# Kernel tuning notes

Measured on AMD Instinct MI355X. Metric: run time of the kernel, lower is better.

The kernel has to match this reference:

```python
import jax, jax.numpy as jnp
import numpy as np

B, T, K, H, NH = 16, 2048, 128, 1024, 8
NEG = -jnp.inf


def _ln(x, g, b, eps=1e-5):
    m = x.mean(-1, keepdims=True)
    v = ((x - m) ** 2).mean(-1, keepdims=True)
    return (x - m) * jax.lax.rsqrt(v + eps) * g + b


def _mha(q, k, v, in_w, in_b, out_w, out_b, nh, bias):
    # torch nn.MultiheadAttention (batch_first, eval mode). bias: additive mask (B or 1, 1, Lq, Lk)
    Bq, Lq, Hd = q.shape
    Lk = k.shape[1]
    d = Hd // nh
    wq, wk, wv = in_w[:Hd], in_w[Hd:2 * Hd], in_w[2 * Hd:]
    bq, bk, bv = in_b[:Hd], in_b[Hd:2 * Hd], in_b[2 * Hd:]
    qh = (q @ wq.T + bq).reshape(Bq, Lq, nh, d).transpose(0, 2, 1, 3)
    kh = (k @ wk.T + bk).reshape(Bq, Lk, nh, d).transpose(0, 2, 1, 3)
    vh = (v @ wv.T + bv).reshape(Bq, Lk, nh, d).transpose(0, 2, 1, 3)
    scores = jnp.einsum('bhqd,bhkd->bhqk', qh, kh) * (1.0 / np.sqrt(d)) + bias
    attn = jax.nn.softmax(scores, axis=-1)
    o = jnp.einsum('bhqk,bhkd->bhqd', attn, vh).transpose(0, 2, 1, 3).reshape(Bq, Lq, Hd)
    return o @ out_w.T + out_b


def setup_inputs() -> dict:
    key = jax.random.key(0)
    ks = jax.random.split(key, 12)
    projected = jax.random.normal(ks[0], (B, T, H), dtype=jnp.float32)
    starts = jnp.sort(jax.random.randint(ks[1], (B, K), 0, T - 1), axis=-1)
    widths = jax.random.randint(ks[2], (B, K), 1, 33)
    ends = jnp.minimum(starts + widths, T)
    boundaries = jnp.stack([starts, ends], axis=-1).astype(jnp.int64)
    slot_mask = jnp.ones((B, K), dtype=jnp.float32)
    s = 0.02
    p = {
        'qp_w': jax.random.normal(ks[3], (H, H)) * s, 'qp_b': jnp.zeros((H,)),
        'ca_in_w': jax.random.normal(ks[4], (3 * H, H)) * s, 'ca_in_b': jnp.zeros((3 * H,)),
        'ca_out_w': jax.random.normal(ks[5], (H, H)) * s, 'ca_out_b': jnp.zeros((H,)),
        'cn_g': jnp.ones((H,)), 'cn_b': jnp.zeros((H,)),
        'sa_in_w': jax.random.normal(ks[6], (3 * H, H)) * s, 'sa_in_b': jnp.zeros((3 * H,)),
        'sa_out_w': jax.random.normal(ks[7], (H, H)) * s, 'sa_out_b': jnp.zeros((H,)),
        'on_g': jnp.ones((H,)), 'on_b': jnp.zeros((H,)),
    }
    return {'projected': projected, 'boundaries': boundaries, 'slot_mask': slot_mask, **p}


def reference(projected, boundaries, slot_mask, qp_w, qp_b, ca_in_w, ca_in_b, ca_out_w, ca_out_b,
              cn_g, cn_b, sa_in_w, sa_in_b, sa_out_w, sa_out_b, on_g, on_b):
    Bb, Tt, Hh = projected.shape
    Kk = slot_mask.shape[1]
    tidx = jnp.arange(Tt)
    starts = boundaries[:, :, 0]  # (B,K)
    ends = boundaries[:, :, 1]
    # in-boundary membership: (B,K,T)
    in_bkt = (tidx[None, None, :] >= starts[:, :, None]) & (tidx[None, None, :] < ends[:, :, None])
    valid = slot_mask > 0.5  # (B,K)
    # --- mean-pool init queries ---
    in_slot = (in_bkt & (slot_mask[:, :, None] > 0)).astype(projected.dtype)  # (B,K,T)
    w = in_slot / jnp.clip(in_slot.sum(axis=-1, keepdims=True), 1.0, None)
    init_slots = jnp.einsum('bkt,bth->bkh', w, projected)
    queries = init_slots @ qp_w.T + qp_b
    # --- boundary-masked cross attention (True = blocked) ---
    blocked = ~(in_bkt & valid[:, :, None])  # (B,K,T)
    cross_bias = jnp.where(blocked, NEG, 0.0)[:, None, :, :]  # (B,1,K,T)
    attn_out = _mha(queries, projected, projected, ca_in_w, ca_in_b, ca_out_w, ca_out_b, NH, cross_bias)
    slots = _ln(attn_out + queries, cn_g, cn_b)
    # --- causal self-attention over slots with key padding ---
    causal = jnp.where(jnp.triu(jnp.ones((Kk, Kk), bool), 1), NEG, 0.0)[None, None, :, :]
    pad = jnp.where(slot_mask[:, None, None, :] < 0.5, NEG, 0.0)  # (B,1,1,K)
    ctx = _mha(slots, slots, slots, sa_in_w, sa_in_b, sa_out_w, sa_out_b, NH, causal + pad)
    return _ln(ctx + slots, on_g, on_b)
```

## Files before the change

kernel.cpp:

```cpp
#include <hip/hip_runtime.h>
#include <hip/hip_bf16.h>


#define Bc 16
#define Tc 2048
#define Kc 128
#define Hc 1024
#define NHc 8

typedef unsigned short u16;
typedef __attribute__((ext_vector_type(8))) short short8v;
typedef __attribute__((ext_vector_type(4))) float f32x4;

__device__ __forceinline__ float bf2f(u16 u){ return __uint_as_float(((unsigned)u)<<16); }
__device__ __forceinline__ u16 f2bf(float f){
  unsigned x = __float_as_uint(f);
  return (u16)((x + 0x7fffu + ((x>>16)&1u)) >> 16);
}
__device__ __forceinline__ float4 ld4(const float* p){ return *(const float4*)p; }
__device__ __forceinline__ float ldx(const void* x, size_t idx, bool isbf){
  return isbf ? bf2f(((const u16*)x)[idx]) : ((const float*)x)[idx];
}
__device__ __forceinline__ bool probe_bf(const u16* probe){ return probe[0] == 0x3F80; }

__device__ __forceinline__ void gload_lds16(const u16* g, u16* l){
  __builtin_amdgcn_global_load_lds(
      (const __attribute__((address_space(1))) unsigned int*)g,
      (__attribute__((address_space(3))) unsigned int*)l, 16, 0, 0);
}

struct CvtArgs { const void* src[15]; int n[15]; long long off[15]; int tobf[15]; };

__global__ __launch_bounds__(256) void convert_params(CvtArgs a, float* fbase,
                                                      u16* bbase, const u16* probe)
{
  bool isbf = probe_bf(probe);
  int g = blockIdx.x*256 + threadIdx.x;
  int stride = gridDim.x*256;
  #pragma unroll 1
  for (int seg=0; seg<15; seg++){
    int n = a.n[seg];
    const void* s = a.src[seg];
    if (a.tobf[seg]){
      u16* d = bbase + a.off[seg];
      if (isbf){ const u16* su=(const u16*)s; for (int i=g;i<n;i+=stride) d[i]=su[i]; }
      else     { const float* sf=(const float*)s; for (int i=g;i<n;i+=stride) d[i]=f2bf(sf[i]); }
    } else {
      float* d = fbase + a.off[seg];
      for (int i=g;i<n;i+=stride) d[i] = ldx(s, i, isbf);
    }
  }
}

__global__ __launch_bounds__(256) void transpose_bf(
    const u16* __restrict__ src, u16* __restrict__ dst, int n)
{
  __shared__ u16 t[32][33];
  int bx = blockIdx.x*32, by = blockIdx.y*32;
  int tx = threadIdx.x & 31, ty = threadIdx.x >> 5;
  #pragma unroll
  for (int i=0;i<32;i+=8)
    t[ty+i][tx] = src[(size_t)(by+ty+i)*n + bx+tx];
  __syncthreads();
  #pragma unroll
  for (int i=0;i<32;i+=8)
    dst[(size_t)(bx+ty+i)*n + by+tx] = t[tx][ty+i];
}

__global__ __launch_bounds__(256) void gemm_mfma(
    const u16* __restrict__ A, const u16* __restrict__ W,
    const float* __restrict__ bias, float* __restrict__ Cf, u16* __restrict__ Cb,
    int M, int N, int Kd, int lda, int ldw, int ldc, float alpha,
    int ZH, long long sAb, long long sAh, long long sWb, long long sWh,
    long long sCb, long long sCh, long long sBh)
{
  __shared__ __align__(16) u16 As[128*32];
  __shared__ __align__(16) u16 Bs[128*32];
  int z = blockIdx.z, bi = z / ZH, hi = z % ZH;
  A += (size_t)bi*sAb + (size_t)hi*sAh;
  W += (size_t)bi*sWb + (size_t)hi*sWh;
  int tid = threadIdx.x;
  int m0 = blockIdx.y*128, n0 = blockIdx.x*128;
  int wave = tid >> 6, lane = tid & 63;
  int wm = (wave >> 1)*64, wn = (wave & 1)*64;
  int r = lane & 15, half = lane >> 4;
  int srow = wave*32 + (lane >> 2);
  int skc  = (lane & 3) << 3;
  u16* ldsA = &As[wave*1024];
  u16* ldsB = &Bs[wave*1024];

  f32x4 acc[4][4] = {};

  for (int k0 = 0; k0 < Kd; k0 += 32){
    gload_lds16(A + (size_t)(m0+srow   )*lda + k0 + skc, ldsA);
    gload_lds16(A + (size_t)(m0+srow+16)*lda + k0 + skc, ldsA + 512);
    gload_lds16(W + (size_t)(n0+srow   )*ldw + k0 + skc, ldsB);
    gload_lds16(W + (size_t)(n0+srow+16)*ldw + k0 + skc, ldsB + 512);
    __syncthreads();
    short8v a[4], b[4];
    #pragma unroll
    for (int mi=0;mi<4;mi++)
      a[mi] = *(const short8v*)&As[(wm+mi*16+r)*32 + half*8];
    #pragma unroll
    for (int ni=0;ni<4;ni++)
      b[ni] = *(const short8v*)&Bs[(wn+ni*16+r)*32 + half*8];
    #pragma unroll
    for (int mi=0;mi<4;mi++)
      #pragma unroll
      for (int ni=0;ni<4;ni++)
        acc[mi][ni] = __builtin_amdgcn_mfma_f32_16x16x32_bf16(a[mi], b[ni], acc[mi][ni], 0, 0, 0);
    __syncthreads();
  }

  float* Cfp = Cf ? Cf + (size_t)bi*sCb + (size_t)hi*sCh : nullptr;
  u16*   Cbp = Cb ? Cb + (size_t)bi*sCb + (size_t)hi*sCh : nullptr;
  #pragma unroll
  for (int ni=0;ni<4;ni++){
    int col = n0 + wn + ni*16 + r;
    float bvv = bias ? bias[(size_t)hi*sBh + col] : 0.f;
    #pragma unroll
    for (int mi=0;mi<4;mi++){
      #pragma unroll
      for (int d=0;d<4;d++){
        int rowc = m0 + wm + mi*16 + half*4 + d;
        float o = alpha*acc[mi][ni][d] + bvv;
        if (Cfp) Cfp[(size_t)rowc*ldc + col] = o;
        if (Cbp) Cbp[(size_t)rowc*ldc + col] = f2bf(o);
      }
    }
  }
}

__global__ __launch_bounds__(256) void gemm_nt(
    const float* __restrict__ A, const float* __restrict__ W,
    const float* __restrict__ bias, float* __restrict__ C,
    int M, int N, int Kd, int lda, int ldw, int ldc, float alpha,
    int ZH, long long sAb, long long sAh, long long sWb, long long sWh,
    long long sCb, long long sCh, long long sBh)
{
  __shared__ float As[16][68];
  __shared__ float Bs[16][68];
  int z = blockIdx.z, bi = z / ZH, hi = z % ZH;
  A += (size_t)bi*sAb + (size_t)hi*sAh;
  W += (size_t)bi*sWb + (size_t)hi*sWh;
  C += (size_t)bi*sCb + (size_t)hi*sCh;
  int tid = threadIdx.x;
  int m0 = blockIdx.y*64, n0 = blockIdx.x*64;
  int tx = tid & 15, ty = tid >> 4;
  int lRow = tid >> 2, lK = (tid & 3) << 2;
  float acc[4][4] = {};
  for (int k0=0; k0<Kd; k0+=16){
    float4 av = ld4(A + (size_t)(m0+lRow)*lda + k0 + lK);
    float4 wv = ld4(W + (size_t)(n0+lRow)*ldw + k0 + lK);
    As[lK+0][lRow]=av.x; As[lK+1][lRow]=av.y; As[lK+2][lRow]=av.z; As[lK+3][lRow]=av.w;
    Bs[lK+0][lRow]=wv.x; Bs[lK+1][lRow]=wv.y; Bs[lK+2][lRow]=wv.z; Bs[lK+3][lRow]=wv.w;
    __syncthreads();
    #pragma unroll
    for (int kk=0;kk<16;kk++){
      float a[4], b[4];
      #pragma unroll
      for (int i=0;i<4;i++) a[i]=As[kk][ty*4+i];
      #pragma unroll
      for (int j=0;j<4;j++) b[j]=Bs[kk][tx*4+j];
      #pragma unroll
      for (int i=0;i<4;i++)
        #pragma unroll
        for (int j=0;j<4;j++)
          acc[i][j] += a[i]*b[j];
    }
    __syncthreads();
  }
  float bv[4] = {0.f,0.f,0.f,0.f};
  if (bias){
    const float* bp = bias + (size_t)hi*sBh + n0 + tx*4;
    bv[0]=bp[0]; bv[1]=bp[1]; bv[2]=bp[2]; bv[3]=bp[3];
  }
  #pragma unroll
  for (int i=0;i<4;i++){
    float4 o;
    o.x = alpha*acc[i][0]+bv[0];
    o.y = alpha*acc[i][1]+bv[1];
    o.z = alpha*acc[i][2]+bv[2];
    o.w = alpha*acc[i][3]+bv[3];
    *(float4*)(C + (size_t)(m0+ty*4+i)*ldc + n0 + tx*4) = o;
  }
}

__global__ __launch_bounds__(256) void gemm_nn(
    const float* __restrict__ A, const float* __restrict__ Bm,
    const float* __restrict__ bias, float* __restrict__ C, u16* __restrict__ Cb,
    int M, int N, int Kd, int lda, int ldb, int ldc, float alpha,
    int ZH, long long sAb, long long sAh, long long sBb, long long sBh,
    long long sCb, long long sCh, long long sBiash)
{
  __shared__ float As[16][68];
  __shared__ float Bs[16][68];
  int z = blockIdx.z, bi = z / ZH, hi = z % ZH;
  A  += (size_t)bi*sAb + (size_t)hi*sAh;
  Bm += (size_t)bi*sBb + (size_t)hi*sBh;
  int tid = threadIdx.x;
  int m0 = blockIdx.y*64, n0 = blockIdx.x*64;
  int tx = tid & 15, ty = tid >> 4;
  int lRow = tid >> 2, lK = (tid & 3) << 2;
  int bKr = tid >> 4, bNc = (tid & 15) << 2;
  float acc[4][4] = {};
  for (int k0=0; k0<Kd; k0+=16){
    float4 av = ld4(A + (size_t)(m0+lRow)*lda + k0 + lK);
    float4 bvv = ld4(Bm + (size_t)(k0+bKr)*ldb + n0 + bNc);
    As[lK+0][lRow]=av.x; As[lK+1][lRow]=av.y; As[lK+2][lRow]=av.z; As[lK+3][lRow]=av.w;
    *(float4*)&Bs[bKr][bNc] = bvv;
    __syncthreads();
    #pragma unroll
    for (int kk=0;kk<16;kk++){
      float a[4], b[4];
      #pragma unroll
      for (int i=0;i<4;i++) a[i]=As[kk][ty*4+i];
      #pragma unroll
      for (int j=0;j<4;j++) b[j]=Bs[kk][tx*4+j];
      #pragma unroll
      for (int i=0;i<4;i++)
        #pragma unroll
        for (int j=0;j<4;j++)
          acc[i][j] += a[i]*b[j];
    }
    __syncthreads();
  }
  float bv[4] = {0.f,0.f,0.f,0.f};
  if (bias){
    const float* bp = bias + (size_t)hi*sBiash + n0 + tx*4;
    bv[0]=bp[0]; bv[1]=bp[1]; bv[2]=bp[2]; bv[3]=bp[3];
  }
  #pragma unroll
  for (int i=0;i<4;i++){
    float o0 = alpha*acc[i][0]+bv[0];
    float o1 = alpha*acc[i][1]+bv[1];
    float o2 = alpha*acc[i][2]+bv[2];
    float o3 = alpha*acc[i][3]+bv[3];
    size_t rowoff = (size_t)(m0+ty*4+i)*ldc + n0 + tx*4;
    if (Cb){
      u16* cp = Cb + (size_t)bi*sCb + (size_t)hi*sCh + rowoff;
      ushort4 ov; ov.x=f2bf(o0); ov.y=f2bf(o1); ov.z=f2bf(o2); ov.w=f2bf(o3);
      *(ushort4*)cp = ov;
    } else {
      float* cp = C + (size_t)bi*sCb + (size_t)hi*sCh + rowoff;
      float4 ov; ov.x=o0; ov.y=o1; ov.z=o2; ov.w=o3;
      *(float4*)cp = ov;
    }
  }
}

__global__ __launch_bounds__(256) void pool_kernel(
    const void* __restrict__ x, const int* __restrict__ bnd,
    const float* __restrict__ maskf, u16* __restrict__ out,
    const u16* __restrict__ probe)
{
  bool isbf = probe_bf(probe);
  bool is64 = (bnd[1] == 0);
  int slot = blockIdx.x; int b = slot >> 7; int tid = threadIdx.x;
  int s0 = is64 ? bnd[4*slot]   : bnd[2*slot];
  int e0 = is64 ? bnd[4*slot+2] : bnd[2*slot+1];
  int d0 = tid*4;
  float acc[4] = {0.f,0.f,0.f,0.f};
  for (int t=s0; t<e0; t++){
    size_t base = ((size_t)b*Tc + (size_t)t)*Hc + d0;
    if (isbf){
      ushort4 v = *(const ushort4*)((const u16*)x + base);
      acc[0]+=bf2f(v.x); acc[1]+=bf2f(v.y); acc[2]+=bf2f(v.z); acc[3]+=bf2f(v.w);
    } else {
      float4 v = ld4((const float*)x + base);
      acc[0]+=v.x; acc[1]+=v.y; acc[2]+=v.z; acc[3]+=v.w;
    }
  }
  int cnt = e0 - s0; if (cnt < 1) cnt = 1;
  float inv = (maskf[slot] > 0.5f) ? 1.f/(float)cnt : 0.f;
  ushort4 o;
  o.x=f2bf(acc[0]*inv); o.y=f2bf(acc[1]*inv); o.z=f2bf(acc[2]*inv); o.w=f2bf(acc[3]*inv);
  *(ushort4*)(out + (size_t)slot*Hc + d0) = o;
}

__global__ __launch_bounds__(512, 2) void cross_attn3(
    const void* __restrict__ x, const int* __restrict__ bnd,
    const u16* __restrict__ Yg, u16* __restrict__ pooled,
    const u16* __restrict__ probe)
{
  __shared__ __align__(16) u16 Xs[32*1024];
  __shared__ float sc[8*32];
  __shared__ __align__(16) float pt[32*8];
  bool isbf = probe_bf(probe);
  bool is64 = (bnd[1] == 0);
  int slot = blockIdx.x; int b = slot >> 7;
  int tid = threadIdx.x;
  int wv = tid >> 6, lane = tid & 63;
  int s0 = is64 ? bnd[4*slot]   : bnd[2*slot];
  int e0 = is64 ? bnd[4*slot+2] : bnd[2*slot+1];
  int w = e0 - s0;

  {
    int rrow = tid >> 7;
    int c = (tid & 127) * 8;
    for (int t = rrow; t < w; t += 4){
      size_t base = ((size_t)b*Tc + (size_t)(s0+t))*Hc + c;
      if (isbf){
        *(short8v*)&Xs[t*1024 + c] = *(const short8v*)((const u16*)x + base);
      } else {
        const float* xf = (const float*)x + base;
        float4 f0 = ld4(xf), f1 = ld4(xf+4);
        short8v v;
        v[0]=(short)f2bf(f0.x); v[1]=(short)f2bf(f0.y);
        v[2]=(short)f2bf(f0.z); v[3]=(short)f2bf(f0.w);
        v[4]=(short)f2bf(f1.x); v[5]=(short)f2bf(f1.y);
        v[6]=(short)f2bf(f1.z); v[7]=(short)f2bf(f1.w);
        *(short8v*)&Xs[t*1024 + c] = v;
      }
    }
  }

  int h = wv;
  float y0[8], y1[8];
  #pragma unroll
  for (int r=0;r<8;r++){
    unsigned yw = *(const unsigned*)(Yg + (size_t)slot*8192 + h*1024 + lane*2 + 128*r);
    y0[r] = bf2f((u16)(yw & 0xffffu));
    y1[r] = bf2f((u16)(yw >> 16));
  }
  __syncthreads();

  const float scale = 0.08838834764831845f;
  for (int t=0; t<w; t++){
    float acc = 0.f;
    #pragma unroll
    for (int r=0;r<8;r++){
      unsigned xw = *(const unsigned*)&Xs[t*1024 + lane*2 + 128*r];
      acc += y0[r]*bf2f((u16)(xw & 0xffffu)) + y1[r]*bf2f((u16)(xw >> 16));
    }
    for (int off=32; off; off>>=1) acc += __shfl_xor(acc, off);
    if (lane==0) sc[h*32 + t] = acc*scale;
  }
  __syncthreads();

  if (tid < 256){
    int hh = tid >> 5, t = tid & 31;
    float v = (t < w) ? sc[hh*32 + t] : -1e30f;
    float m = v;
    for (int off=16; off; off>>=1) m = fmaxf(m, __shfl_xor(m, off));
    float e = (t < w) ? __expf(v - m) : 0.f;
    float s = e;
    for (int off=16; off; off>>=1) s += __shfl_xor(s, off);
    pt[t*8 + hh] = e / s;
  }
  __syncthreads();

  {
    int d0 = tid*2;
    float pa[8][2] = {};
    for (int t=0; t<w; t++){
      float4 p0 = *(const float4*)&pt[t*8];
      float4 p1 = *(const float4*)&pt[t*8+4];
      unsigned xw = *(const unsigned*)&Xs[t*1024 + d0];
      float x0 = bf2f((u16)(xw & 0xffffu));
      float x1 = bf2f((u16)(xw >> 16));
      pa[0][0]+=p0.x*x0; pa[0][1]+=p0.x*x1;
      pa[1][0]+=p0.y*x0; pa[1][1]+=p0.y*x1;
      pa[2][0]+=p0.z*x0; pa[2][1]+=p0.z*x1;
      pa[3][0]+=p0.w*x0; pa[3][1]+=p0.w*x1;
      pa[4][0]+=p1.x*x0; pa[4][1]+=p1.x*x1;
      pa[5][0]+=p1.y*x0; pa[5][1]+=p1.y*x1;
      pa[6][0]+=p1.z*x0; pa[6][1]+=p1.z*x1;
      pa[7][0]+=p1.w*x0; pa[7][1]+=p1.w*x1;
    }
    #pragma unroll
    for (int hh=0;hh<8;hh++){
      ushort2 o; o.x = f2bf(pa[hh][0]); o.y = f2bf(pa[hh][1]);
      *(ushort2*)(pooled + (size_t)slot*8192 + hh*1024 + d0) = o;
    }
  }
}

__global__ __launch_bounds__(256) void ln_res(
    const float* __restrict__ xin, const float* __restrict__ res,
    const float* __restrict__ g, const float* __restrict__ bb,
    float* __restrict__ outf, u16* __restrict__ outb, const u16* __restrict__ probe,
    u16* __restrict__ dualb)
{
  __shared__ float red[256];
  bool tobf = (probe != nullptr) && probe_bf(probe);
  int row = blockIdx.x, tid = threadIdx.x;
  const float* xr = xin + (size_t)row*1024;
  const float* rr = res + (size_t)row*1024;
  float v[4]; float s = 0.f;
  #pragma unroll
  for (int r=0;r<4;r++){ v[r] = xr[tid+256*r] + rr[tid+256*r]; s += v[r]; }
  red[tid] = s; __syncthreads();
  for (int off=128; off>0; off>>=1){ if (tid<off) red[tid]+=red[tid+off]; __syncthreads(); }
  float mean = red[0] * (1.f/1024.f);
  __syncthreads();
  float s2 = 0.f;
  #pragma unroll
  for (int r=0;r<4;r++){ float d = v[r]-mean; s2 += d*d; }
  red[tid]=s2; __syncthreads();
  for (int off=128; off>0; off>>=1){ if (tid<off) red[tid]+=red[tid+off]; __syncthreads(); }
  float var = red[0]*(1.f/1024.f);
  float rs = rsqrtf(var + 1e-5f);
  #pragma unroll
  for (int r=0;r<4;r++){
    int c = tid+256*r;
    float o = (v[r]-mean)*rs*g[c] + bb[c];
    if (tobf) outb[(size_t)row*1024 + c] = f2bf(o);
    else      outf[(size_t)row*1024 + c] = o;
    if (dualb) dualb[(size_t)row*1024 + c] = f2bf(o);
  }
}

__global__ __launch_bounds__(256) void sa_softmax(float* __restrict__ S,
                                                  const float* __restrict__ maskf)
{
  int wv = threadIdx.x>>6, lane = threadIdx.x&63;
  int row = blockIdx.x*4 + wv;
  int z = row >> 7, q = row & 127;
  int b = z >> 3;
  float* Sr = S + (size_t)row*128;
  float v0 = Sr[lane], v1 = Sr[lane+64];
  if (lane    > q || maskf[b*128+lane   ] < 0.5f) v0 = -1e30f;
  if (lane+64 > q || maskf[b*128+lane+64] < 0.5f) v1 = -1e30f;
  float m = fmaxf(v0,v1);
  for (int off=32; off; off>>=1) m = fmaxf(m, __shfl_xor(m,off));
  float e0 = expf(v0-m), e1 = expf(v1-m);
  float s = e0+e1;
  for (int off=32; off; off>>=1) s += __shfl_xor(s,off);
  float inv = 1.f/s;
  Sr[lane] = e0*inv; Sr[lane+64] = e1*inv;
}

extern "C" void kernel_launch(void* const* d_in, const int* in_sizes, int n_in,
                              void* d_out, int out_size, void* d_ws, size_t ws_size,
                              hipStream_t stream)
{
  const void* x       = d_in[0];
  const int* bnd      = (const int*)d_in[1];
  const u16* probe    = (const u16*)d_in[9];
  float* ws = (float*)d_ws;

  const long long F_qp_b    = 0;
  const long long F_ca_in_b = 1024;
  const long long F_ca_out_b= 4096;
  const long long F_cn_g    = 5120;
  const long long F_cn_b    = 6144;
  const long long F_sa_in_b = 7168;
  const long long F_sa_out_b= 10240;
  const long long F_on_g    = 11264;
  const long long F_on_b    = 12288;
  const long long F_smask   = 13312;
  u16* wb = (u16*)(ws + 15360);
  const long long B_qp_w    = 0;
  const long long B_ca_in_w = 1048576;
  const long long B_ca_out_w= 4194304;
  const long long B_sa_in_w = 5242880;
  const long long B_sa_out_w= 8388608;
  const long long B_wkT     = 9437184;
  const long long PB        = 5258240;

  float* qbuf    = ws + PB + 0;
  float* slots   = ws + PB + 2097152;
  u16*   Ybuf    = (u16*)(ws + PB + 4194304);
  u16*   poolb   = Ybuf;
  u16*   islots  = (u16*)(ws + PB + 12582912);
  u16*   qbuf_b  = (u16*)(ws + PB + 13631488);
  u16*   qhbuf   = (u16*)(ws + PB + 14680064);
  u16*   attnb   = (u16*)(ws + PB + 15728640);
  float* attn2   = ws + PB + 16777216;
  u16*   slots_b = (u16*)(ws + PB + 18874368);
  float* qkv     = ws + PB + 19922944;
  float* Sb      = ws + PB + 26214400;
  u16*   ctx_b   = (u16*)(ws + PB + 28311552);
  float* ctx2    = ws + PB + 29360128;
  if (ws_size < (size_t)(PB + 31457280ll) * 4ull) return;

  CvtArgs ca;
  const int srcIdx[15]     = {3,5,7,11,13, 4,6,8,9,10,12,14,15,16, 2};
  const long long offs[15] = {B_qp_w,B_ca_in_w,B_ca_out_w,B_sa_in_w,B_sa_out_w,
                              F_qp_b,F_ca_in_b,F_ca_out_b,F_cn_g,F_cn_b,
                              F_sa_in_b,F_sa_out_b,F_on_g,F_on_b,F_smask};
  const int tobf[15]       = {1,1,1,1,1, 0,0,0,0,0,0,0,0,0, 0};
  for (int i=0;i<15;i++){ ca.src[i]=d_in[srcIdx[i]]; ca.n[i]=in_sizes[srcIdx[i]];
                          ca.off[i]=offs[i]; ca.tobf[i]=tobf[i]; }
  convert_params<<<dim3(4096),dim3(256),0,stream>>>(ca, ws, wb, probe);

  const float* Pf = ws;
  transpose_bf<<<dim3(32,32),dim3(256),0,stream>>>(wb + B_ca_in_w + 1048576ll,
      wb + B_wkT, 1024);
  pool_kernel<<<dim3(2048),dim3(256),0,stream>>>(x, bnd, Pf+F_smask, islots, probe);
  gemm_mfma<<<dim3(8,16,1),dim3(256),0,stream>>>(islots, wb+B_qp_w, Pf+F_qp_b,
      qbuf, qbuf_b,
      2048,1024,1024, 1024,1024,1024, 1.f, 1, 0,0, 0,0, 0,0, 0);
  gemm_mfma<<<dim3(8,16,1),dim3(256),0,stream>>>(qbuf_b, wb+B_ca_in_w, Pf+F_ca_in_b,
      (float*)nullptr, qhbuf,
      2048,1024,1024, 1024,1024,1024, 1.f, 1, 0,0, 0,0, 0,0, 0);
  gemm_mfma<<<dim3(8,16,8),dim3(256),0,stream>>>(qhbuf, wb+B_wkT,
      (const float*)nullptr, (float*)nullptr, Ybuf,
      2048,1024,128, 1024,1024,8192, 1.f, 8, 0,128, 0,128, 0,1024, 0);
  cross_attn3<<<dim3(2048),dim3(512),0,stream>>>(x, bnd, Ybuf, poolb, probe);
  gemm_mfma<<<dim3(1,16,8),dim3(256),0,stream>>>(poolb, wb+B_ca_in_w+2097152ll,
      Pf+F_ca_in_b+2048, (float*)nullptr, attnb,
      2048,128,1024, 8192,1024,1024, 1.f, 8, 0,1024, 0,131072, 0,128, 128);
  gemm_mfma<<<dim3(8,16,1),dim3(256),0,stream>>>(attnb, wb+B_ca_out_w, Pf+F_ca_out_b,
      attn2, (u16*)nullptr,
      2048,1024,1024, 1024,1024,1024, 1.f, 1, 0,0, 0,0, 0,0, 0);
  ln_res<<<dim3(2048),dim3(256),0,stream>>>(attn2, qbuf, Pf+F_cn_g, Pf+F_cn_b,
      slots, (u16*)nullptr, (const u16*)nullptr, slots_b);
  gemm_mfma<<<dim3(24,16,1),dim3(256),0,stream>>>(slots_b, wb+B_sa_in_w, Pf+F_sa_in_b,
      qkv, (u16*)nullptr,
      2048,3072,1024, 1024,1024,3072, 1.f, 1, 0,0, 0,0, 0,0, 0);
  gemm_nt<<<dim3(2,2,128),dim3(256),0,stream>>>(qkv, qkv + 1024,
      (const float*)nullptr, Sb,
      128,128,128, 3072,3072,128, 0.08838834764831845f, 8,
      393216,128, 393216,128, 131072,16384, 0);
  sa_softmax<<<dim3(4096),dim3(256),0,stream>>>(Sb, Pf+F_smask);
  gemm_nn<<<dim3(2,2,128),dim3(256),0,stream>>>(Sb, qkv + 2048,
      (const float*)nullptr, (float*)nullptr, ctx_b,
      128,128,128, 128,3072,1024, 1.f, 8,
      131072,16384, 393216,128, 131072,128, 0);
  gemm_mfma<<<dim3(8,16,1),dim3(256),0,stream>>>(ctx_b, wb+B_sa_out_w, Pf+F_sa_out_b,
      ctx2, (u16*)nullptr,
      2048,1024,1024, 1024,1024,1024, 1.f, 1, 0,0, 0,0, 0,0, 0);
  ln_res<<<dim3(2048),dim3(256),0,stream>>>(ctx2, slots, Pf+F_on_g, Pf+F_on_b,
      (float*)d_out, (u16*)d_out, probe, (u16*)nullptr);
}
```

Before: 567.7 us.

## Compute cross-attention scores with MFMA on swizzled LDS and split pooling rows

New measurement: 538.7 us. 5.1% less time.

```diff
diff --git a/kernel.cpp b/kernel.cpp
--- a/kernel.cpp
+++ b/kernel.cpp
@@ -249,19 +249,21 @@
   }
 }
 
-__global__ __launch_bounds__(256) void pool_kernel(
+__global__ __launch_bounds__(512) void pool_kernel(
     const void* __restrict__ x, const int* __restrict__ bnd,
     const float* __restrict__ maskf, u16* __restrict__ out,
     const u16* __restrict__ probe)
 {
+  __shared__ float red[1024];
   bool isbf = probe_bf(probe);
   bool is64 = (bnd[1] == 0);
   int slot = blockIdx.x; int b = slot >> 7; int tid = threadIdx.x;
   int s0 = is64 ? bnd[4*slot]   : bnd[2*slot];
   int e0 = is64 ? bnd[4*slot+2] : bnd[2*slot+1];
-  int d0 = tid*4;
+  int rh = tid >> 8;
+  int d0 = (tid & 255)*4;
   float acc[4] = {0.f,0.f,0.f,0.f};
-  for (int t=s0; t<e0; t++){
+  for (int t=s0+rh; t<e0; t+=2){
     size_t base = ((size_t)b*Tc + (size_t)t)*Hc + d0;
     if (isbf){
       ushort4 v = *(const ushort4*)((const u16*)x + base);
@@ -271,19 +273,30 @@
       acc[0]+=v.x; acc[1]+=v.y; acc[2]+=v.z; acc[3]+=v.w;
     }
   }
-  int cnt = e0 - s0; if (cnt < 1) cnt = 1;
-  float inv = (maskf[slot] > 0.5f) ? 1.f/(float)cnt : 0.f;
-  ushort4 o;
-  o.x=f2bf(acc[0]*inv); o.y=f2bf(acc[1]*inv); o.z=f2bf(acc[2]*inv); o.w=f2bf(acc[3]*inv);
-  *(ushort4*)(out + (size_t)slot*Hc + d0) = o;
-}
-
-__global__ __launch_bounds__(512, 2) void cross_attn3(
+  if (rh == 1){
+    #pragma unroll
+    for (int r=0;r<4;r++) red[(tid&255)*4 + r] = acc[r];
+  }
+  __syncthreads();
+  if (rh == 0){
+    int cnt = e0 - s0; if (cnt < 1) cnt = 1;
+    float inv = (maskf[slot] > 0.5f) ? 1.f/(float)cnt : 0.f;
+    ushort4 o;
+    o.x=f2bf((acc[0]+red[(tid&255)*4+0])*inv);
+    o.y=f2bf((acc[1]+red[(tid&255)*4+1])*inv);
+    o.z=f2bf((acc[2]+red[(tid&255)*4+2])*inv);
+    o.w=f2bf((acc[3]+red[(tid&255)*4+3])*inv);
+    *(ushort4*)(out + (size_t)slot*Hc + d0) = o;
+  }
+}
+
+__global__ __launch_bounds__(512, 2) void cross_attn4(
     const void* __restrict__ x, const int* __restrict__ bnd,
     const u16* __restrict__ Yg, u16* __restrict__ pooled,
     const u16* __restrict__ probe)
 {
   __shared__ __align__(16) u16 Xs[32*1024];
+  __shared__ float redC[4*2*64*4];
   __shared__ float sc[8*32];
   __shared__ __align__(16) float pt[32*8];
   bool isbf = probe_bf(probe);
@@ -297,44 +310,57 @@
 
   {
     int rrow = tid >> 7;
-    int c = (tid & 127) * 8;
+    int cu = (tid & 127) * 8;
     for (int t = rrow; t < w; t += 4){
-      size_t base = ((size_t)b*Tc + (size_t)(s0+t))*Hc + c;
+      size_t base = ((size_t)b*Tc + (size_t)(s0+t))*Hc + cu;
+      int dst = t*1024 + (cu ^ ((t&7)<<3));
+      short8v v;
       if (isbf){
-        *(short8v*)&Xs[t*1024 + c] = *(const short8v*)((const u16*)x + base);
+        v = *(const short8v*)((const u16*)x + base);
       } else {
         const float* xf = (const float*)x + base;
         float4 f0 = ld4(xf), f1 = ld4(xf+4);
-        short8v v;
         v[0]=(short)f2bf(f0.x); v[1]=(short)f2bf(f0.y);
         v[2]=(short)f2bf(f0.z); v[3]=(short)f2bf(f0.w);
         v[4]=(short)f2bf(f1.x); v[5]=(short)f2bf(f1.y);
         v[6]=(short)f2bf(f1.z); v[7]=(short)f2bf(f1.w);
-        *(short8v*)&Xs[t*1024 + c] = v;
       }
-    }
-  }
-
-  int h = wv;
-  float y0[8], y1[8];
-  #pragma unroll
-  for (int r=0;r<8;r++){
-    unsigned yw = *(const unsigned*)(Yg + (size_t)slot*8192 + h*1024 + lane*2 + 128*r);
-    y0[r] = bf2f((u16)(yw & 0xffffu));
-    y1[r] = bf2f((u16)(yw >> 16));
-  }
-  __syncthreads();
-
-  const float scale = 0.08838834764831845f;
-  for (int t=0; t<w; t++){
-    float acc = 0.f;
-    #pragma unroll
-    for (int r=0;r<8;r++){
-      unsigned xw = *(const unsigned*)&Xs[t*1024 + lane*2 + 128*r];
-      acc += y0[r]*bf2f((u16)(xw & 0xffffu)) + y1[r]*bf2f((u16)(xw >> 16));
-    }
-    for (int off=32; off; off>>=1) acc += __shfl_xor(acc, off);
-    if (lane==0) sc[h*32 + t] = acc*scale;
+      *(short8v*)&Xs[dst] = v;
+    }
+  }
+  __syncthreads();
+
+  if (wv < 4){
+    int r = lane & 15, half = lane >> 4;
+    f32x4 acc0 = {0.f,0.f,0.f,0.f}, acc1 = {0.f,0.f,0.f,0.f};
+    #pragma unroll
+    for (int ks=0; ks<8; ks++){
+      int k = wv*256 + ks*32 + half*8;
+      short8v vb = {0,0,0,0,0,0,0,0};
+      if (r < 8)
+        vb = *(const short8v*)(Yg + (size_t)slot*8192 + r*1024 + k);
+      int xs = k ^ ((r&7)<<3);
+      short8v a0 = *(const short8v*)&Xs[ r      *1024 + xs];
+      short8v a1 = *(const short8v*)&Xs[(16+r)*1024 + xs];
+      acc0 = __builtin_amdgcn_mfma_f32_16x16x32_bf16(a0, vb, acc0, 0, 0, 0);
+      acc1 = __builtin_amdgcn_mfma_f32_16x16x32_bf16(a1, vb, acc1, 0, 0, 0);
+    }
+    #pragma unroll
+    for (int i=0;i<4;i++){
+      redC[((wv*2+0)*64+lane)*4+i] = acc0[i];
+      redC[((wv*2+1)*64+lane)*4+i] = acc1[i];
+    }
+  }
+  __syncthreads();
+
+  {
+    int f = tid >> 8, rem = tid & 255, l = rem >> 2, i = rem & 3;
+    float v = 0.f;
+    #pragma unroll
+    for (int q=0; q<4; q++) v += redC[((q*2+f)*64+l)*4+i];
+    int hh = l & 15;
+    int t  = f*16 + (l>>4)*4 + i;
+    if (hh < 8) sc[hh*32 + t] = v * 0.08838834764831845f;
   }
   __syncthreads();
 
@@ -356,7 +382,7 @@
     for (int t=0; t<w; t++){
       float4 p0 = *(const float4*)&pt[t*8];
       float4 p1 = *(const float4*)&pt[t*8+4];
-      unsigned xw = *(const unsigned*)&Xs[t*1024 + d0];
+      unsigned xw = *(const unsigned*)&Xs[t*1024 + (d0 ^ ((t&7)<<3))];
       float x0 = bf2f((u16)(xw & 0xffffu));
       float x1 = bf2f((u16)(xw >> 16));
       pa[0][0]+=p0.x*x0; pa[0][1]+=p0.x*x1;
@@ -488,7 +514,7 @@
   const float* Pf = ws;
   transpose_bf<<<dim3(32,32),dim3(256),0,stream>>>(wb + B_ca_in_w + 1048576ll,
       wb + B_wkT, 1024);
-  pool_kernel<<<dim3(2048),dim3(256),0,stream>>>(x, bnd, Pf+F_smask, islots, probe);
+  pool_kernel<<<dim3(2048),dim3(512),0,stream>>>(x, bnd, Pf+F_smask, islots, probe);
   gemm_mfma<<<dim3(8,16,1),dim3(256),0,stream>>>(islots, wb+B_qp_w, Pf+F_qp_b,
       qbuf, qbuf_b,
       2048,1024,1024, 1024,1024,1024, 1.f, 1, 0,0, 0,0, 0,0, 0);
@@ -498,7 +524,7 @@
   gemm_mfma<<<dim3(8,16,8),dim3(256),0,stream>>>(qhbuf, wb+B_wkT,
       (const float*)nullptr, (float*)nullptr, Ybuf,
       2048,1024,128, 1024,1024,8192, 1.f, 8, 0,128, 0,128, 0,1024, 0);
-  cross_attn3<<<dim3(2048),dim3(512),0,stream>>>(x, bnd, Ybuf, poolb, probe);
+  cross_attn4<<<dim3(2048),dim3(512),0,stream>>>(x, bnd, Ybuf, poolb, probe);
   gemm_mfma<<<dim3(1,16,8),dim3(256),0,stream>>>(poolb, wb+B_ca_in_w+2097152ll,
       Pf+F_ca_in_b+2048, (float*)nullptr, attnb,
       2048,128,1024, 8192,1024,1024, 1.f, 8, 0,1024, 0,131072, 0,128, 128);
```
